# Performance work log

Measured on AMD Instinct MI355X. Metric: run time of the kernel, lower is better.

Reference implementation:

```python
import jax, jax.numpy as jnp
import numpy as np

NOVELTY_WEIGHT = 2.0
EPS = 1e-8  # torch cosine_similarity eps


def setup_inputs() -> dict:
    key = jax.random.key(0)
    k1, k2, k3, k4 = jax.random.split(key, 4)
    N, M, D = 8192, 8192, 512
    return {
        "predictions": jax.random.normal(k1, (N,), dtype=jnp.float32),
        "targets": jax.random.uniform(k2, (N,), dtype=jnp.float32),
        "features": jax.random.normal(k3, (N, D), dtype=jnp.float32),
        "memory_features": jax.random.normal(k4, (M, D), dtype=jnp.float32),
    }


def reference(predictions, targets, features, memory_features):
    # BCE-with-logits, reduction='none': softplus(x) - x*t
    base_loss = jax.nn.softplus(predictions) - predictions * targets  # [N]

    # Cosine similarity features[N,D] vs memory[M,D]: normalize + GEMM
    f_norm = jnp.maximum(jnp.linalg.norm(features, axis=1, keepdims=True), EPS)
    m_norm = jnp.maximum(jnp.linalg.norm(memory_features, axis=1, keepdims=True), EPS)
    sims = jnp.einsum("nd,md->nm", features / f_norm, memory_features / m_norm)  # [N, M]

    max_sims = jnp.max(sims, axis=1)          # [N]
    novelty_scores = 1.0 - max_sims           # [N]
    novelty_weights = 1.0 + NOVELTY_WEIGHT * novelty_scores

    return jnp.mean(base_loss * novelty_weights)
```

## Files before the change

### kernel.cpp

```cpp
#include <hip/hip_runtime.h>
#include <math.h>

typedef unsigned char u8;
typedef unsigned short u16;
typedef unsigned int u32;
typedef __attribute__((ext_vector_type(8))) int i32x8;
typedef __attribute__((ext_vector_type(4))) float f32x4;

#define SC1 0x7F7F7F7F
#define CPB 1024
#define NCT (CPB / 128)


__device__ __forceinline__ u32 ordf(float f) {
    u32 u = __float_as_uint(f);
    return (u & 0x80000000u) ? ~u : (u | 0x80000000u);
}
__device__ __forceinline__ float unordf(u32 u) {
    u = (u & 0x80000000u) ? (u & 0x7FFFFFFFu) : ~u;
    return __uint_as_float(u);
}

__device__ __forceinline__ u32 f2e4m3(float x) {
    u32 u = __float_as_uint(x);
    u32 sgn = (u >> 24) & 0x80u;
    int ne = (int)((u >> 23) & 0xFF) - 120;
    if (ne >= 1) {
        u32 m = u & 0x7FFFFFu;
        u32 keep = m >> 20;
        u32 rest = m & 0xFFFFFu;
        keep += (rest > 0x80000u) || (rest == 0x80000u && (keep & 1u));
        if (keep == 8u) { keep = 0u; ne += 1; }
        return sgn | ((u32)ne << 3) | keep;
    }
    float ax = __uint_as_float(u & 0x7FFFFFFFu);
    u32 f = (u32)__builtin_rintf(ax * 512.0f);
    if (f >= 8u) return sgn | 0x08u;
    return sgn | f;
}

__device__ __forceinline__ void gload_lds16(const void* gsrc, void* ldst) {
    __builtin_amdgcn_global_load_lds(
        (const __attribute__((address_space(1))) void*)gsrc,
        (__attribute__((address_space(3))) void*)ldst,
        16, 0, 0);
}

__device__ __forceinline__ i32x8 ldfrag(const char* plo, const char* phi) {
    int4 lo = *(const int4*)plo;
    int4 hi = *(const int4*)phi;
    i32x8 r = {lo.x, lo.y, lo.z, lo.w, hi.x, hi.y, hi.z, hi.w};
    return r;
}

#define BARRIER do { __builtin_amdgcn_sched_barrier(0); \
                     __builtin_amdgcn_s_barrier(); \
                     __builtin_amdgcn_sched_barrier(0); } while (0)
#define VMCNT(n) do { asm volatile("s_waitcnt vmcnt(" #n ")" ::: "memory"); \
                      __builtin_amdgcn_sched_barrier(0); } while (0)


__global__ __launch_bounds__(256) void norm_kernel(
    const float* __restrict__ feat, const float* __restrict__ memf,
    u8* __restrict__ fb, u8* __restrict__ mb, u32* __restrict__ rowmax,
    int N, int M, int D)
{
    const int lane = threadIdx.x & 63;
    const int wid  = threadIdx.x >> 6;
    const int rid  = blockIdx.x * 4 + wid;
    if (rid >= N + M) return;

    const float* src;
    u8* dst;
    if (rid < N) { src = feat + (size_t)rid * D; dst = fb + (size_t)rid * D; }
    else         { src = memf + (size_t)(rid - N) * D; dst = mb + (size_t)(rid - N) * D; }

    float4 v0 = *(const float4*)(src + lane * 8);
    float4 v1 = *(const float4*)(src + lane * 8 + 4);
    float ss = v0.x*v0.x + v0.y*v0.y + v0.z*v0.z + v0.w*v0.w
             + v1.x*v1.x + v1.y*v1.y + v1.z*v1.z + v1.w*v1.w;
    #pragma unroll
    for (int m = 1; m <= 32; m <<= 1) ss += __shfl_xor(ss, m);

    float inv = 1.0f / fmaxf(sqrtf(ss), 1e-8f);

    u32 w0 =  f2e4m3(v0.x * inv)        | (f2e4m3(v0.y * inv) << 8)
           | (f2e4m3(v0.z * inv) << 16) | (f2e4m3(v0.w * inv) << 24);
    u32 w1 =  f2e4m3(v1.x * inv)        | (f2e4m3(v1.y * inv) << 8)
           | (f2e4m3(v1.z * inv) << 16) | (f2e4m3(v1.w * inv) << 24);
    *(uint2*)(dst + lane * 8) = make_uint2(w0, w1);

    if (rid < N && lane == 0) rowmax[rid] = 0u;
}


#define STAGE_B(gB) do { \
    _Pragma("unroll") \
    for (int kt_ = 0; kt_ < 4; ++kt_) \
      _Pragma("unroll") \
      for (int p_ = 0; p_ < 4; ++p_) \
        gload_lds16((gB) + (size_t)(p_ * 32) * D + kt_ * 128, \
                    &L[kt_ * 16384 + p_ * 4096 + tid * 16]); \
  } while (0)

__global__ __launch_bounds__(256, 2) void gemm_max_kernel(
    const u8* __restrict__ fb, const u8* __restrict__ mb,
    u32* __restrict__ rowmax, int N, int M, int D)
{
    __shared__ __align__(16) u8 L[65536];

    const int tid  = threadIdx.x;
    const int lane = tid & 63;
    const int wid  = tid >> 6;
    const int wwr  = wid >> 1;
    const int wwc  = wid & 1;
    const int l15  = lane & 15;
    const int l4   = lane >> 4;
    const int n0   = blockIdx.y * 128;
    const int m0   = blockIdx.x * CPB;

    const int t8   = tid >> 3;
    const int swz  = ((tid & 7) ^ (t8 & 7)) * 16;

    const int s    = (l15 & 7) << 4;
    const int oLo  = (l4 * 32) ^ s;
    const int oHi  = (l4 * 32 + 16) ^ s;
    const char* Lb = (const char*)L;
    const char* Bbase = Lb + (wwc * 64 + l15) * 128;

    const u8* gB0 = mb + (size_t)(m0 + t8) * D + swz;
    STAGE_B(gB0);

    const u8* gArow = fb + (size_t)(n0 + wwr * 64 + l15) * D + l4 * 32;
    i32x8 areg[4][4];
    #pragma unroll
    for (int i = 0; i < 4; ++i)
        #pragma unroll
        for (int kt = 0; kt < 4; ++kt)
            areg[i][kt] = *(const i32x8*)(gArow + (size_t)(i * 16) * D + kt * 128);

    VMCNT(0);
    BARRIER;

    f32x4 acc[4][4] = {};
    float vmax[4][4];
    #pragma unroll
    for (int i = 0; i < 4; ++i)
        #pragma unroll
        for (int rr = 0; rr < 4; ++rr) vmax[i][rr] = -1e30f;

    for (int ct = 0; ct < NCT; ++ct) {
        if (ct > 0) {
            BARRIER;
            const u8* gB = mb + (size_t)(m0 + ct * 128 + t8) * D + swz;
            STAGE_B(gB);
            VMCNT(0);
            BARRIER;
        }

        #pragma unroll
        for (int kt = 0; kt < 4; ++kt) {
            #pragma unroll
            for (int j = 0; j < 4; ++j) {
                i32x8 bfj = ldfrag(Bbase + kt * 16384 + j * 2048 + oLo,
                                   Bbase + kt * 16384 + j * 2048 + oHi);
                #pragma unroll
                for (int i = 0; i < 4; ++i)
                    acc[i][j] = __builtin_amdgcn_mfma_scale_f32_16x16x128_f8f6f4(
                        areg[i][kt], bfj, acc[i][j], 0, 0, 0, SC1, 0, SC1);
            }
        }

        #pragma unroll
        for (int i = 0; i < 4; ++i)
            #pragma unroll
            for (int rr = 0; rr < 4; ++rr) {
                float v = fmaxf(fmaxf(acc[i][0][rr], acc[i][1][rr]),
                                fmaxf(acc[i][2][rr], acc[i][3][rr]));
                vmax[i][rr] = fmaxf(vmax[i][rr], v);
            }
        #pragma unroll
        for (int i = 0; i < 4; ++i)
            #pragma unroll
            for (int j = 0; j < 4; ++j) acc[i][j] = (f32x4)0.0f;
    }

    BARRIER;
    float* red = (float*)L;
    #pragma unroll
    for (int i = 0; i < 4; ++i) {
        #pragma unroll
        for (int rr = 0; rr < 4; ++rr) {
            float v = vmax[i][rr];
            v = fmaxf(v, __shfl_xor(v, 1));
            v = fmaxf(v, __shfl_xor(v, 2));
            v = fmaxf(v, __shfl_xor(v, 4));
            v = fmaxf(v, __shfl_xor(v, 8));
            if (l15 == 0) {
                int rloc = wwr * 64 + i * 16 + l4 * 4 + rr;
                red[rloc * 2 + wwc] = v;
            }
        }
    }
    __syncthreads();
    if (tid < 128) {
        float v = fmaxf(red[tid * 2 + 0], red[tid * 2 + 1]);
        atomicMax(&rowmax[n0 + tid], ordf(v));
    }
}


__global__ __launch_bounds__(256) void finalize1_kernel(
    const float* __restrict__ pred, const float* __restrict__ targ,
    const u32* __restrict__ rowmax, float* __restrict__ partial, int N)
{
    __shared__ float ws4[4];
    const int tid = threadIdx.x;
    const int i = blockIdx.x * 256 + tid;

    float sv = 0.f;
    if (i < N) {
        float x = pred[i];
        float t = targ[i];
        float bl = fmaxf(x, 0.f) + log1pf(expf(-fabsf(x))) - x * t;
        float ms = unordf(rowmax[i]);
        sv = bl * (1.0f + 2.0f * (1.0f - ms));
    }
    #pragma unroll
    for (int m = 1; m <= 32; m <<= 1) sv += __shfl_xor(sv, m);
    if ((tid & 63) == 0) ws4[tid >> 6] = sv;
    __syncthreads();
    if (tid == 0) partial[blockIdx.x] = ws4[0] + ws4[1] + ws4[2] + ws4[3];
}


__global__ __launch_bounds__(64) void finalize2_kernel(
    const float* __restrict__ partial, float* __restrict__ out, int nb, int N)
{
    float sv = 0.f;
    for (int i = threadIdx.x; i < nb; i += 64) sv += partial[i];
    #pragma unroll
    for (int m = 1; m <= 32; m <<= 1) sv += __shfl_xor(sv, m);
    if (threadIdx.x == 0) out[0] = sv / (float)N;
}


extern "C" void kernel_launch(void* const* d_in, const int* in_sizes, int n_in,
                              void* d_out, int out_size, void* d_ws, size_t ws_size,
                              hipStream_t stream) {
    const float* pred = (const float*)d_in[0];
    const float* targ = (const float*)d_in[1];
    const float* feat = (const float*)d_in[2];
    const float* memf = (const float*)d_in[3];
    const int N = in_sizes[0];
    const int D = in_sizes[2] / N;
    const int M = in_sizes[3] / D;
    float* out = (float*)d_out;

    u8* fb8 = (u8*)d_ws;
    u8* mb8 = fb8 + (size_t)N * D;
    u32* rowmax = (u32*)(mb8 + (size_t)M * D);
    float* partial = (float*)(rowmax + N);

    const int rows = N + M;
    const int nb = (N + 255) / 256;
    norm_kernel<<<dim3((rows + 3) / 4), dim3(256), 0, stream>>>(
        feat, memf, fb8, mb8, rowmax, N, M, D);
    gemm_max_kernel<<<dim3(M / CPB, N / 128), dim3(256), 0, stream>>>(
        fb8, mb8, rowmax, N, M, D);
    finalize1_kernel<<<dim3(nb), dim3(256), 0, stream>>>(
        pred, targ, rowmax, partial, N);
    finalize2_kernel<<<dim3(1), dim3(64), 0, stream>>>(partial, out, nb, N);
}
```

Measured before the change: 50.22 us.

## Double-buffer B tiles in LDS and enlarge per-block A tile to 256 rows

The GEMM-max kernel now keeps 256 feature rows per block in registers, with 128 per wave-row. It streams 64-row memory tiles through two 32KB LDS buffers, prefetching the next tile while computing the current one and waiting with a partial vmcnt. This is meant to hide global-to-LDS load latency and double A-fragment reuse per B tile. The cost is twice the A registers, launch bounds cut to one block per CU, and half as many blocks in the grid, which lowers occupancy.

```diff
diff --git a/kernel.cpp b/kernel.cpp
--- a/kernel.cpp
+++ b/kernel.cpp
@@ -2,14 +2,13 @@
 #include <math.h>
 
 typedef unsigned char u8;
-typedef unsigned short u16;
 typedef unsigned int u32;
 typedef __attribute__((ext_vector_type(8))) int i32x8;
 typedef __attribute__((ext_vector_type(4))) float f32x4;
 
 #define SC1 0x7F7F7F7F
 #define CPB 1024
-#define NCT (CPB / 128)
+#define NCT 16
 
 
 __device__ __forceinline__ u32 ordf(float f) {
@@ -94,16 +93,16 @@
 }
 
 
-#define STAGE_B(gB) do { \
+#define STAGE_B(ct, bufo) do { \
     _Pragma("unroll") \
-    for (int kt_ = 0; kt_ < 4; ++kt_) \
-      _Pragma("unroll") \
-      for (int p_ = 0; p_ < 4; ++p_) \
-        gload_lds16((gB) + (size_t)(p_ * 32) * D + kt_ * 128, \
-                    &L[kt_ * 16384 + p_ * 4096 + tid * 16]); \
-  } while (0)
-
-__global__ __launch_bounds__(256, 2) void gemm_max_kernel(
+    for (int kt_ = 0; kt_ < 4; ++kt_) { \
+      gload_lds16(gBs + (size_t)(ct) * 64 * D + kt_ * 128, \
+                  &L[(bufo) + kt_ * 8192 + tid * 16]); \
+      gload_lds16(gBs + (size_t)(ct) * 64 * D + (size_t)32 * D + kt_ * 128, \
+                  &L[(bufo) + kt_ * 8192 + 4096 + tid * 16]); \
+    } } while (0)
+
+__global__ __launch_bounds__(256, 1) void gemm_max_kernel(
     const u8* __restrict__ fb, const u8* __restrict__ mb,
     u32* __restrict__ rowmax, int N, int M, int D)
 {
@@ -116,79 +115,76 @@
     const int wwc  = wid & 1;
     const int l15  = lane & 15;
     const int l4   = lane >> 4;
-    const int n0   = blockIdx.y * 128;
+    const int n0   = blockIdx.y * 256;
     const int m0   = blockIdx.x * CPB;
 
-    const int t8   = tid >> 3;
-    const int swz  = ((tid & 7) ^ (t8 & 7)) * 16;
-
-    const int s    = (l15 & 7) << 4;
-    const int oLo  = (l4 * 32) ^ s;
-    const int oHi  = (l4 * 32 + 16) ^ s;
+    const int srow   = tid >> 3;
+    const int schunk = (tid & 7) ^ (srow & 7);
+    const u8* gBs = mb + (size_t)(m0 + srow) * D + schunk * 16;
+
+    const int s   = (l15 & 7) << 4;
+    const int oLo = (l4 * 32) ^ s;
+    const int oHi = (l4 * 32 + 16) ^ s;
     const char* Lb = (const char*)L;
-    const char* Bbase = Lb + (wwc * 64 + l15) * 128;
-
-    const u8* gB0 = mb + (size_t)(m0 + t8) * D + swz;
-    STAGE_B(gB0);
-
-    const u8* gArow = fb + (size_t)(n0 + wwr * 64 + l15) * D + l4 * 32;
-    i32x8 areg[4][4];
-    #pragma unroll
-    for (int i = 0; i < 4; ++i)
+    const int rdoff = (wwc * 32 + l15) * 128;
+
+    STAGE_B(0, 0);
+
+    const u8* gA = fb + (size_t)(n0 + wwr * 128 + l15) * D + l4 * 32;
+    i32x8 areg[8][4];
+    #pragma unroll
+    for (int i = 0; i < 8; ++i)
         #pragma unroll
         for (int kt = 0; kt < 4; ++kt)
-            areg[i][kt] = *(const i32x8*)(gArow + (size_t)(i * 16) * D + kt * 128);
-
-    VMCNT(0);
-    BARRIER;
-
-    f32x4 acc[4][4] = {};
-    float vmax[4][4];
-    #pragma unroll
-    for (int i = 0; i < 4; ++i)
+            areg[i][kt] = *(const i32x8*)(gA + (size_t)(i * 16) * D + kt * 128);
+
+    f32x4 acc[8][2] = {};
+    float vmax[8][4];
+    #pragma unroll
+    for (int i = 0; i < 8; ++i)
         #pragma unroll
         for (int rr = 0; rr < 4; ++rr) vmax[i][rr] = -1e30f;
 
+    #pragma unroll 2
     for (int ct = 0; ct < NCT; ++ct) {
-        if (ct > 0) {
-            BARRIER;
-            const u8* gB = mb + (size_t)(m0 + ct * 128 + t8) * D + swz;
-            STAGE_B(gB);
-            VMCNT(0);
-            BARRIER;
-        }
-
+        const int cur = (ct & 1) * 32768;
+
+        BARRIER;
+        if (ct + 1 < NCT) { STAGE_B(ct + 1, 32768 - cur); VMCNT(8); }
+        else              { VMCNT(0); }
+        BARRIER;
+
+        const char* Bt = Lb + cur + rdoff;
         #pragma unroll
         for (int kt = 0; kt < 4; ++kt) {
+            i32x8 bf0 = ldfrag(Bt + kt * 8192 + oLo,        Bt + kt * 8192 + oHi);
+            i32x8 bf1 = ldfrag(Bt + kt * 8192 + 2048 + oLo, Bt + kt * 8192 + 2048 + oHi);
             #pragma unroll
-            for (int j = 0; j < 4; ++j) {
-                i32x8 bfj = ldfrag(Bbase + kt * 16384 + j * 2048 + oLo,
-                                   Bbase + kt * 16384 + j * 2048 + oHi);
-                #pragma unroll
-                for (int i = 0; i < 4; ++i)
-                    acc[i][j] = __builtin_amdgcn_mfma_scale_f32_16x16x128_f8f6f4(
-                        areg[i][kt], bfj, acc[i][j], 0, 0, 0, SC1, 0, SC1);
+            for (int i = 0; i < 8; ++i) {
+                acc[i][0] = __builtin_amdgcn_mfma_scale_f32_16x16x128_f8f6f4(
+                    areg[i][kt], bf0, acc[i][0], 0, 0, 0, SC1, 0, SC1);
+                acc[i][1] = __builtin_amdgcn_mfma_scale_f32_16x16x128_f8f6f4(
+                    areg[i][kt], bf1, acc[i][1], 0, 0, 0, SC1, 0, SC1);
             }
         }
 
         #pragma unroll
-        for (int i = 0; i < 4; ++i)
+        for (int i = 0; i < 8; ++i)
             #pragma unroll
-            for (int rr = 0; rr < 4; ++rr) {
-                float v = fmaxf(fmaxf(acc[i][0][rr], acc[i][1][rr]),
-                                fmaxf(acc[i][2][rr], acc[i][3][rr]));
-                vmax[i][rr] = fmaxf(vmax[i][rr], v);
-            }
-        #pragma unroll
-        for (int i = 0; i < 4; ++i)
-            #pragma unroll
-            for (int j = 0; j < 4; ++j) acc[i][j] = (f32x4)0.0f;
+            for (int rr = 0; rr < 4; ++rr)
+                vmax[i][rr] = fmaxf(vmax[i][rr],
+                                    fmaxf(acc[i][0][rr], acc[i][1][rr]));
+        #pragma unroll
+        for (int i = 0; i < 8; ++i) {
+            acc[i][0] = (f32x4)0.0f;
+            acc[i][1] = (f32x4)0.0f;
+        }
     }
 
     BARRIER;
     float* red = (float*)L;
     #pragma unroll
-    for (int i = 0; i < 4; ++i) {
+    for (int i = 0; i < 8; ++i) {
         #pragma unroll
         for (int rr = 0; rr < 4; ++rr) {
             float v = vmax[i][rr];
@@ -197,13 +193,13 @@
             v = fmaxf(v, __shfl_xor(v, 4));
             v = fmaxf(v, __shfl_xor(v, 8));
             if (l15 == 0) {
-                int rloc = wwr * 64 + i * 16 + l4 * 4 + rr;
+                int rloc = wwr * 128 + i * 16 + l4 * 4 + rr;
                 red[rloc * 2 + wwc] = v;
             }
         }
     }
     __syncthreads();
-    if (tid < 128) {
+    if (tid < 256) {
         float v = fmaxf(red[tid * 2 + 0], red[tid * 2 + 1]);
         atomicMax(&rowmax[n0 + tid], ordf(v));
     }
@@ -266,7 +262,7 @@
     const int nb = (N + 255) / 256;
     norm_kernel<<<dim3((rows + 3) / 4), dim3(256), 0, stream>>>(
         feat, memf, fb8, mb8, rowmax, N, M, D);
-    gemm_max_kernel<<<dim3(M / CPB, N / 128), dim3(256), 0, stream>>>(
+    gemm_max_kernel<<<dim3(M / CPB, N / 256), dim3(256), 0, stream>>>(
         fb8, mb8, rowmax, N, M, D);
     finalize1_kernel<<<dim3(nb), dim3(256), 0, stream>>>(
         pred, targ, rowmax, partial, N);
```

Result: slower. 57.46 us (+14.4%).

## Load B fragments directly from global into registers with software pipelining, drop LDS staging

Applied to the files above, without the earlier changes.

Removes the LDS staging of memory-feature tiles (global_load_lds plus barriers) and has each wave load its B fragments straight from global memory into registers. Loads are double-buffered across K-steps so the next fragment load overlaps the current MFMAs. This drops the block barriers and LDS traffic, but each wave now fetches B independently. B reuse across the two row-waves then depends on L1/L2 instead of shared memory, and the global access pattern is less coalesced.

```diff
diff --git a/kernel.cpp b/kernel.cpp
--- a/kernel.cpp
+++ b/kernel.cpp
@@ -2,14 +2,13 @@
 #include <math.h>
 
 typedef unsigned char u8;
-typedef unsigned short u16;
 typedef unsigned int u32;
 typedef __attribute__((ext_vector_type(8))) int i32x8;
 typedef __attribute__((ext_vector_type(4))) float f32x4;
 
 #define SC1 0x7F7F7F7F
 #define CPB 1024
-#define NCT (CPB / 128)
+#define NCT 8
 
 
 __device__ __forceinline__ u32 ordf(float f) {
@@ -39,26 +38,6 @@
     return sgn | f;
 }
 
-__device__ __forceinline__ void gload_lds16(const void* gsrc, void* ldst) {
-    __builtin_amdgcn_global_load_lds(
-        (const __attribute__((address_space(1))) void*)gsrc,
-        (__attribute__((address_space(3))) void*)ldst,
-        16, 0, 0);
-}
-
-__device__ __forceinline__ i32x8 ldfrag(const char* plo, const char* phi) {
-    int4 lo = *(const int4*)plo;
-    int4 hi = *(const int4*)phi;
-    i32x8 r = {lo.x, lo.y, lo.z, lo.w, hi.x, hi.y, hi.z, hi.w};
-    return r;
-}
-
-#define BARRIER do { __builtin_amdgcn_sched_barrier(0); \
-                     __builtin_amdgcn_s_barrier(); \
-                     __builtin_amdgcn_sched_barrier(0); } while (0)
-#define VMCNT(n) do { asm volatile("s_waitcnt vmcnt(" #n ")" ::: "memory"); \
-                      __builtin_amdgcn_sched_barrier(0); } while (0)
-
 
 __global__ __launch_bounds__(256) void norm_kernel(
     const float* __restrict__ feat, const float* __restrict__ memf,
@@ -94,20 +73,26 @@
 }
 
 
-#define STAGE_B(gB) do { \
+#define LDB(v0, v1, ct, kt, h) do { \
+    const u8* p_ = gBw + (size_t)(((ct) * 128 + (h) * 32)) * D + (kt) * 128; \
+    v0 = *(const i32x8*)(p_); \
+    v1 = *(const i32x8*)(p_ + (size_t)16 * D); \
+  } while (0)
+
+#define MM(v0, v1, kt, h) do { \
     _Pragma("unroll") \
-    for (int kt_ = 0; kt_ < 4; ++kt_) \
-      _Pragma("unroll") \
-      for (int p_ = 0; p_ < 4; ++p_) \
-        gload_lds16((gB) + (size_t)(p_ * 32) * D + kt_ * 128, \
-                    &L[kt_ * 16384 + p_ * 4096 + tid * 16]); \
-  } while (0)
+    for (int i_ = 0; i_ < 4; ++i_) { \
+      acc[i_][(h)*2]   = __builtin_amdgcn_mfma_scale_f32_16x16x128_f8f6f4( \
+          areg[i_][kt], v0, acc[i_][(h)*2],   0, 0, 0, SC1, 0, SC1); \
+      acc[i_][(h)*2+1] = __builtin_amdgcn_mfma_scale_f32_16x16x128_f8f6f4( \
+          areg[i_][kt], v1, acc[i_][(h)*2+1], 0, 0, 0, SC1, 0, SC1); \
+    } } while (0)
 
 __global__ __launch_bounds__(256, 2) void gemm_max_kernel(
     const u8* __restrict__ fb, const u8* __restrict__ mb,
     u32* __restrict__ rowmax, int N, int M, int D)
 {
-    __shared__ __align__(16) u8 L[65536];
+    __shared__ float red[256];
 
     const int tid  = threadIdx.x;
     const int lane = tid & 63;
@@ -119,28 +104,15 @@
     const int n0   = blockIdx.y * 128;
     const int m0   = blockIdx.x * CPB;
 
-    const int t8   = tid >> 3;
-    const int swz  = ((tid & 7) ^ (t8 & 7)) * 16;
-
-    const int s    = (l15 & 7) << 4;
-    const int oLo  = (l4 * 32) ^ s;
-    const int oHi  = (l4 * 32 + 16) ^ s;
-    const char* Lb = (const char*)L;
-    const char* Bbase = Lb + (wwc * 64 + l15) * 128;
-
-    const u8* gB0 = mb + (size_t)(m0 + t8) * D + swz;
-    STAGE_B(gB0);
-
-    const u8* gArow = fb + (size_t)(n0 + wwr * 64 + l15) * D + l4 * 32;
+    const u8* gA = fb + (size_t)(n0 + wwr * 64 + l15) * D + l4 * 32;
     i32x8 areg[4][4];
     #pragma unroll
     for (int i = 0; i < 4; ++i)
         #pragma unroll
         for (int kt = 0; kt < 4; ++kt)
-            areg[i][kt] = *(const i32x8*)(gArow + (size_t)(i * 16) * D + kt * 128);
-
-    VMCNT(0);
-    BARRIER;
+            areg[i][kt] = *(const i32x8*)(gA + (size_t)(i * 16) * D + kt * 128);
+
+    const u8* gBw = mb + (size_t)(m0 + wwc * 64 + l15) * D + l4 * 32;
 
     f32x4 acc[4][4] = {};
     float vmax[4][4];
@@ -149,27 +121,22 @@
         #pragma unroll
         for (int rr = 0; rr < 4; ++rr) vmax[i][rr] = -1e30f;
 
+    i32x8 P0, P1, Q0, Q1;
+    LDB(P0, P1, 0, 0, 0);
+    LDB(Q0, Q1, 0, 0, 1);
+
+    #pragma unroll 1
     for (int ct = 0; ct < NCT; ++ct) {
-        if (ct > 0) {
-            BARRIER;
-            const u8* gB = mb + (size_t)(m0 + ct * 128 + t8) * D + swz;
-            STAGE_B(gB);
-            VMCNT(0);
-            BARRIER;
-        }
-
-        #pragma unroll
-        for (int kt = 0; kt < 4; ++kt) {
-            #pragma unroll
-            for (int j = 0; j < 4; ++j) {
-                i32x8 bfj = ldfrag(Bbase + kt * 16384 + j * 2048 + oLo,
-                                   Bbase + kt * 16384 + j * 2048 + oHi);
-                #pragma unroll
-                for (int i = 0; i < 4; ++i)
-                    acc[i][j] = __builtin_amdgcn_mfma_scale_f32_16x16x128_f8f6f4(
-                        areg[i][kt], bfj, acc[i][j], 0, 0, 0, SC1, 0, SC1);
-            }
-        }
+        const int cn = (ct + 1 < NCT) ? ct + 1 : ct;
+
+        MM(P0, P1, 0, 0);  LDB(P0, P1, ct, 1, 0);
+        MM(Q0, Q1, 0, 1);  LDB(Q0, Q1, ct, 1, 1);
+        MM(P0, P1, 1, 0);  LDB(P0, P1, ct, 2, 0);
+        MM(Q0, Q1, 1, 1);  LDB(Q0, Q1, ct, 2, 1);
+        MM(P0, P1, 2, 0);  LDB(P0, P1, ct, 3, 0);
+        MM(Q0, Q1, 2, 1);  LDB(Q0, Q1, ct, 3, 1);
+        MM(P0, P1, 3, 0);  LDB(P0, P1, cn, 0, 0);
+        MM(Q0, Q1, 3, 1);  LDB(Q0, Q1, cn, 0, 1);
 
         #pragma unroll
         for (int i = 0; i < 4; ++i)
@@ -185,8 +152,6 @@
             for (int j = 0; j < 4; ++j) acc[i][j] = (f32x4)0.0f;
     }
 
-    BARRIER;
-    float* red = (float*)L;
     #pragma unroll
     for (int i = 0; i < 4; ++i) {
         #pragma unroll
```

New measurement: 105.7 us. 110% more time.
